# Kernel optimization log

Hardware: AMD Instinct MI355X
Metric: run time of the kernel (lower is better)

The kernel has to match this reference:

```python
import jax, jax.numpy as jnp
import numpy as np

NUM_LAYER, BS, NUM_HEADS, INPUT_LEN, ENC_LEN = 4, 2, 16, 1024, 588
HID = 256
LN_EPS = 1e-5


def _ln(x, g, b):
    mu = jnp.mean(x, axis=-1, keepdims=True)
    var = jnp.mean((x - mu) ** 2, axis=-1, keepdims=True)
    return (x - mu) / jnp.sqrt(var + LN_EPS) * g + b


def _mlp(x, Ws, bs, gs, betas):
    # 3-layer LayerNorm -> Linear (+GELU except last)
    n = len(Ws)
    for i in range(n):
        x = _ln(x, gs[i], betas[i])
        x = x @ Ws[i] + bs[i]
        if i < n - 1:
            x = jax.nn.gelu(x, approximate=False)  # torch F.gelu default = exact
    return x


def setup_inputs() -> dict:
    key = jax.random.key(0)
    ks = jax.random.split(key, 24)
    s = 0.02
    dims = [(ENC_LEN, HID), (HID, HID), (HID, 4)]
    inp = {
        "heatmap": jax.random.normal(ks[0], (NUM_LAYER, BS, NUM_HEADS, INPUT_LEN, ENC_LEN), jnp.float32),
        "attention_valid_mask": jnp.ones((BS, INPUT_LEN), jnp.float32),
        "W_head": jax.random.normal(ks[1], (NUM_LAYER * NUM_HEADS, 1), jnp.float32) * s,
        "b_head": jnp.zeros((1,), jnp.float32),
        "W_keep": jax.random.normal(ks[2], (ENC_LEN, 1), jnp.float32) * s,
        "b_keep": jnp.zeros((1,), jnp.float32),
    }
    for br in (1, 2):
        for i, (di, do) in enumerate(dims):
            inp[f"W{br}_{i}"] = jax.random.normal(ks[3 + br * 4 + i], (di, do), jnp.float32) * s
            inp[f"b{br}_{i}"] = jnp.zeros((do,), jnp.float32)
    for i, d in enumerate([ENC_LEN, HID, HID]):
        inp[f"g{i}"] = jnp.ones((d,), jnp.float32)
        inp[f"beta{i}"] = jnp.zeros((d,), jnp.float32)
    return inp


def reference(heatmap, attention_valid_mask, W_head, b_head, W_keep, b_keep,
              W1_0, b1_0, W1_1, b1_1, W1_2, b1_2,
              W2_0, b2_0, W2_1, b2_1, W2_2, b2_2,
              g0, beta0, g1, beta1, g2, beta2):
    num_layer, bs, num_heads, input_len, enc_len = heatmap.shape
    # [L,B,H,T,E] -> [B,T,E,L*H]
    hm = jnp.transpose(heatmap, (1, 3, 4, 0, 2)).reshape(bs, input_len, enc_len, num_layer * num_heads)
    x = (hm @ W_head + b_head)[..., 0]            # [B,T,E]
    x = x.reshape(bs * input_len, enc_len)        # [B*T, 588]
    logits_keep_row = (x @ W_keep + b_keep)[:, 0]  # [B*T]

    gs, betas = [g0, g1, g2], [beta0, beta1, beta2]
    out1 = _mlp(x, [W1_0, W1_1, W1_2], [b1_0, b1_1, b1_2], gs, betas)
    out2 = _mlp(x, [W2_0, W2_1, W2_2], [b2_0, b2_1, b2_2], gs, betas)
    keep = (jax.nn.sigmoid(logits_keep_row) > 0.5)[:, None]  # keep_row_thres = 0.5
    out = jnp.where(keep, out1, out2)             # gather/compute/scatter == select

    out = jax.nn.sigmoid(out.reshape(bs, input_len, 4))
    # input_len != 4095, so the mask-shift branch is skipped
    out = out * attention_valid_mask[:, :, None]
    x1, y1, w, h = out[:, :, 0], out[:, :, 1], out[:, :, 2], out[:, :, 3]
    return (x1, y1, x1 + w, y1 + h, logits_keep_row)
```

## Files before the change

### kernel.cpp

```cpp
#include <hip/hip_runtime.h>
#include <hip/hip_bf16.h>
#include <math.h>

#define NLAYER 4
#define BSZ 2
#define NHEADS 16
#define ILEN 1024
#define ELEN 588
#define HID 256
#define NROWS (BSZ * ILEN)
#define NCH (NLAYER * NHEADS)
#define S_H ((size_t)(ILEN) * ELEN)
#define S_B ((size_t)NHEADS * S_H)
#define S_L ((size_t)BSZ * S_B)

typedef float f32x4 __attribute__((ext_vector_type(4)));

__device__ __forceinline__ float gelu_exact(float x) {
    return 0.5f * x * (1.0f + erff(x * 0.70710678118654752440f));
}
__device__ __forceinline__ float sigmoidf(float x) {
    return 1.0f / (1.0f + expf(-x));
}
__device__ __forceinline__ float wave_sum(float v) {
    #pragma unroll
    for (int m = 1; m < 64; m <<= 1) v += __shfl_xor(v, m);
    return v;
}

__global__ __launch_bounds__(256) void k_reduce_ln0(
    const float* __restrict__ hm, const float* __restrict__ Wh,
    const float* __restrict__ bh, const float* __restrict__ Wk,
    const float* __restrict__ bk, const float* __restrict__ g0,
    const float* __restrict__ be0, float* __restrict__ y,
    float* __restrict__ out_logits)
{
    const int row = blockIdx.x;
    const int b = row >> 10;
    const int i = row & 1023;
    const int tid = threadIdx.x;

    __shared__ float s_wh[NCH];
    __shared__ float s_wk[ELEN];
    __shared__ float s_red[12];
    __shared__ float s_bcast[2];

    if (tid < NCH) s_wh[tid] = Wh[tid];
    for (int e = tid; e < ELEN; e += 256) s_wk[e] = Wk[e];
    __syncthreads();

    const int f4 = tid;
    f32x4 acc = {0.f, 0.f, 0.f, 0.f};

    if (f4 < 147) {
        const float* rowbase = hm + (size_t)b * S_B + (size_t)i * ELEN + (size_t)(f4 * 4);
        #pragma unroll 16
        for (int ch = 0; ch < NCH; ++ch) {
            const size_t off = (size_t)(ch >> 4) * S_L + (size_t)(ch & 15) * S_H;
            const f32x4 v = __builtin_nontemporal_load((const f32x4*)(rowbase + off));
            acc += v * s_wh[ch];
        }
        const float bhv = bh[0];
        acc.x += bhv; acc.y += bhv; acc.z += bhv; acc.w += bhv;
    }

    float sx = 0.f, sxx = 0.f, sk = 0.f;
    if (f4 < 147) {
        sx  = acc.x + acc.y + acc.z + acc.w;
        sxx = acc.x * acc.x + acc.y * acc.y + acc.z * acc.z + acc.w * acc.w;
        const float4 wk = *(const float4*)&s_wk[f4 * 4];
        sk  = acc.x * wk.x + acc.y * wk.y + acc.z * wk.z + acc.w * wk.w;
    }
    #pragma unroll
    for (int off = 32; off; off >>= 1) {
        sx  += __shfl_down(sx, off);
        sxx += __shfl_down(sxx, off);
        sk  += __shfl_down(sk, off);
    }
    const int wid = tid >> 6, lane = tid & 63;
    if (lane == 0) { s_red[wid] = sx; s_red[4 + wid] = sxx; s_red[8 + wid] = sk; }
    __syncthreads();
    if (tid == 0) {
        sx  = s_red[0] + s_red[1] + s_red[2] + s_red[3];
        sxx = s_red[4] + s_red[5] + s_red[6] + s_red[7];
        sk  = s_red[8] + s_red[9] + s_red[10] + s_red[11];
        const float mu   = sx * (1.0f / ELEN);
        const float var  = sxx * (1.0f / ELEN) - mu * mu;
        const float rstd = rsqrtf(var + 1e-5f);
        s_bcast[0] = mu; s_bcast[1] = rstd;
        out_logits[row] = sk + bk[0];
    }
    __syncthreads();
    if (f4 < 147) {
        const float mu = s_bcast[0], rstd = s_bcast[1];
        const float4 gv = *(const float4*)&g0[f4 * 4];
        const float4 bv = *(const float4*)&be0[f4 * 4];
        float4 o;
        o.x = (acc.x - mu) * rstd * gv.x + bv.x;
        o.y = (acc.y - mu) * rstd * gv.y + bv.y;
        o.z = (acc.z - mu) * rstd * gv.z + bv.z;
        o.w = (acc.w - mu) * rstd * gv.w + bv.w;
        *(float4*)&y[(size_t)row * ELEN + f4 * 4] = o;
    }
}

__global__ __launch_bounds__(512) void k_mlp_fused(
    const float* __restrict__ y,
    const float* __restrict__ W10, const float* __restrict__ b10,
    const float* __restrict__ W11, const float* __restrict__ b11,
    const float* __restrict__ W12, const float* __restrict__ b12,
    const float* __restrict__ W20, const float* __restrict__ b20,
    const float* __restrict__ W21, const float* __restrict__ b21,
    const float* __restrict__ W22, const float* __restrict__ b22,
    const float* __restrict__ g1, const float* __restrict__ be1,
    const float* __restrict__ g2, const float* __restrict__ be2,
    const float* __restrict__ mask, float* __restrict__ dout)
{
    __shared__ float y_lds[8][ELEN];
    __shared__ float h_lds[8][HID];

    const int tid  = threadIdx.x;
    const int row0 = blockIdx.x * 8;

    for (int fi = tid; fi < 8 * 147; fi += 512) {
        const int r = fi / 147, t = fi % 147;
        *(float4*)&y_lds[r][t * 4] =
            *(const float4*)&y[(size_t)(row0 + r) * ELEN + t * 4];
    }
    __syncthreads();

    const int w    = tid >> 6;
    const int lane = tid & 63;
    const int col  = lane * 4;
    const int grow = row0 + w;

    const float4 gg1 = *(const float4*)&g1[col];
    const float4 be1v = *(const float4*)&be1[col];
    const float4 gg2 = *(const float4*)&g2[col];
    const float4 be2v = *(const float4*)&be2[col];

    float res[2][4];

    #pragma unroll
    for (int br = 0; br < 2; ++br) {
        const float* W0  = br ? W20 : W10;
        const float* bb0 = br ? b20 : b10;
        const float* W1  = br ? W21 : W11;
        const float* bb1 = br ? b21 : b11;
        const float* W2  = br ? W22 : W12;
        const float* bb2 = br ? b22 : b12;

        float4 a = make_float4(0.f, 0.f, 0.f, 0.f);
        for (int e = 0; e < ELEN; e += 4) {
            const float4 ya = *(const float4*)&y_lds[w][e];
            const float4 w0 = *(const float4*)&W0[(size_t)(e + 0) * HID + col];
            const float4 w1 = *(const float4*)&W0[(size_t)(e + 1) * HID + col];
            const float4 w2 = *(const float4*)&W0[(size_t)(e + 2) * HID + col];
            const float4 w3 = *(const float4*)&W0[(size_t)(e + 3) * HID + col];
            a.x += ya.x * w0.x + ya.y * w1.x + ya.z * w2.x + ya.w * w3.x;
            a.y += ya.x * w0.y + ya.y * w1.y + ya.z * w2.y + ya.w * w3.y;
            a.z += ya.x * w0.z + ya.y * w1.z + ya.z * w2.z + ya.w * w3.z;
            a.w += ya.x * w0.w + ya.y * w1.w + ya.z * w2.w + ya.w * w3.w;
        }
        {
            const float4 bv = *(const float4*)&bb0[col];
            a.x = gelu_exact(a.x + bv.x);
            a.y = gelu_exact(a.y + bv.y);
            a.z = gelu_exact(a.z + bv.z);
            a.w = gelu_exact(a.w + bv.w);
        }
        {
            float s1 = wave_sum(a.x + a.y + a.z + a.w);
            float s2 = wave_sum(a.x * a.x + a.y * a.y + a.z * a.z + a.w * a.w);
            const float mu   = s1 * (1.0f / HID);
            const float rstd = rsqrtf(s2 * (1.0f / HID) - mu * mu + 1e-5f);
            float4 o;
            o.x = (a.x - mu) * rstd * gg1.x + be1v.x;
            o.y = (a.y - mu) * rstd * gg1.y + be1v.y;
            o.z = (a.z - mu) * rstd * gg1.z + be1v.z;
            o.w = (a.w - mu) * rstd * gg1.w + be1v.w;
            *(float4*)&h_lds[w][col] = o;
        }
        float4 c = make_float4(0.f, 0.f, 0.f, 0.f);
        for (int e = 0; e < HID; e += 4) {
            const float4 ha = *(const float4*)&h_lds[w][e];
            const float4 w0 = *(const float4*)&W1[(size_t)(e + 0) * HID + col];
            const float4 w1 = *(const float4*)&W1[(size_t)(e + 1) * HID + col];
            const float4 w2 = *(const float4*)&W1[(size_t)(e + 2) * HID + col];
            const float4 w3 = *(const float4*)&W1[(size_t)(e + 3) * HID + col];
            c.x += ha.x * w0.x + ha.y * w1.x + ha.z * w2.x + ha.w * w3.x;
            c.y += ha.x * w0.y + ha.y * w1.y + ha.z * w2.y + ha.w * w3.y;
            c.z += ha.x * w0.z + ha.y * w1.z + ha.z * w2.z + ha.w * w3.z;
            c.w += ha.x * w0.w + ha.y * w1.w + ha.z * w2.w + ha.w * w3.w;
        }
        {
            const float4 bv = *(const float4*)&bb1[col];
            c.x = gelu_exact(c.x + bv.x);
            c.y = gelu_exact(c.y + bv.y);
            c.z = gelu_exact(c.z + bv.z);
            c.w = gelu_exact(c.w + bv.w);
        }
        float zn[4];
        {
            float s1 = wave_sum(c.x + c.y + c.z + c.w);
            float s2 = wave_sum(c.x * c.x + c.y * c.y + c.z * c.z + c.w * c.w);
            const float mu   = s1 * (1.0f / HID);
            const float rstd = rsqrtf(s2 * (1.0f / HID) - mu * mu + 1e-5f);
            zn[0] = (c.x - mu) * rstd * gg2.x + be2v.x;
            zn[1] = (c.y - mu) * rstd * gg2.y + be2v.y;
            zn[2] = (c.z - mu) * rstd * gg2.z + be2v.z;
            zn[3] = (c.w - mu) * rstd * gg2.w + be2v.w;
        }
        float p[4] = {0.f, 0.f, 0.f, 0.f};
        #pragma unroll
        for (int k = 0; k < 4; ++k) {
            const float4 w4 = *(const float4*)&W2[(size_t)(col + k) * 4];
            p[0] += zn[k] * w4.x;
            p[1] += zn[k] * w4.y;
            p[2] += zn[k] * w4.z;
            p[3] += zn[k] * w4.w;
        }
        #pragma unroll
        for (int cc = 0; cc < 4; ++cc)
            res[br][cc] = wave_sum(p[cc]) + bb2[cc];
    }

    if (lane == 0) {
        const float logit = dout[4 * NROWS + grow];
        const float m = mask[grow];
        const float* sel = (logit > 0.f) ? res[0] : res[1];
        const float x1 = sigmoidf(sel[0]) * m;
        const float y1 = sigmoidf(sel[1]) * m;
        const float ww = sigmoidf(sel[2]) * m;
        const float hh = sigmoidf(sel[3]) * m;
        dout[grow]             = x1;
        dout[NROWS + grow]     = y1;
        dout[2 * NROWS + grow] = x1 + ww;
        dout[3 * NROWS + grow] = y1 + hh;
    }
}

extern "C" void kernel_launch(void* const* d_in, const int* in_sizes, int n_in,
                              void* d_out, int out_size, void* d_ws, size_t ws_size,
                              hipStream_t stream)
{
    const float* hm   = (const float*)d_in[0];
    const float* mask = (const float*)d_in[1];
    const float* Wh   = (const float*)d_in[2];
    const float* bh   = (const float*)d_in[3];
    const float* Wk   = (const float*)d_in[4];
    const float* bk   = (const float*)d_in[5];
    const float* W10  = (const float*)d_in[6];
    const float* b10  = (const float*)d_in[7];
    const float* W11  = (const float*)d_in[8];
    const float* b11  = (const float*)d_in[9];
    const float* W12  = (const float*)d_in[10];
    const float* b12  = (const float*)d_in[11];
    const float* W20  = (const float*)d_in[12];
    const float* b20  = (const float*)d_in[13];
    const float* W21  = (const float*)d_in[14];
    const float* b21  = (const float*)d_in[15];
    const float* W22  = (const float*)d_in[16];
    const float* b22  = (const float*)d_in[17];
    const float* g0   = (const float*)d_in[18];
    const float* be0  = (const float*)d_in[19];
    const float* g1   = (const float*)d_in[20];
    const float* be1  = (const float*)d_in[21];
    const float* g2   = (const float*)d_in[22];
    const float* be2  = (const float*)d_in[23];

    float* ws   = (float*)d_ws;
    float* y    = ws;
    float* dout = (float*)d_out;

    k_reduce_ln0<<<NROWS, 256, 0, stream>>>(hm, Wh, bh, Wk, bk, g0, be0,
                                            y, dout + 4 * NROWS);
    k_mlp_fused<<<NROWS / 8, 512, 0, stream>>>(y, W10, b10, W11, b11, W12, b12,
                                               W20, b20, W21, b21, W22, b22,
                                               g1, be1, g2, be2, mask, dout);
}
```

Before: 547.7 us.

## Process four rows per reduce block, split MLP branches with LDS weight tiles

The reduction kernel now handles four contiguous rows per 640-thread block. This gives each channel load a contiguous 4-row span and cuts the number of blocks, with cross-row statistics gathered through shared-memory partials. The MLP kernel is split so each block computes a single branch for 8 rows, staging weight tiles in LDS and having each wave compute two rows to reuse weights. A third small kernel does the keep/select, sigmoid and masking, at the cost of an extra launch and workspace round trip.

```diff
diff --git a/kernel.cpp b/kernel.cpp
--- a/kernel.cpp
+++ b/kernel.cpp
@@ -28,216 +28,251 @@
     return v;
 }
 
-__global__ __launch_bounds__(256) void k_reduce_ln0(
+__global__ __launch_bounds__(640) void k_reduce_ln0(
     const float* __restrict__ hm, const float* __restrict__ Wh,
     const float* __restrict__ bh, const float* __restrict__ Wk,
     const float* __restrict__ bk, const float* __restrict__ g0,
     const float* __restrict__ be0, float* __restrict__ y,
     float* __restrict__ out_logits)
 {
-    const int row = blockIdx.x;
-    const int b = row >> 10;
-    const int i = row & 1023;
-    const int tid = threadIdx.x;
+    const int row0 = blockIdx.x * 4;
+    const int b    = row0 >> 10;
+    const int i0   = row0 & 1023;
+    const int tid  = threadIdx.x;
 
     __shared__ float s_wh[NCH];
     __shared__ float s_wk[ELEN];
-    __shared__ float s_red[12];
-    __shared__ float s_bcast[2];
+    __shared__ float p_sx[588], p_sxx[588], p_sk[588];
+    __shared__ float s_stat[4][2];
 
     if (tid < NCH) s_wh[tid] = Wh[tid];
-    for (int e = tid; e < ELEN; e += 256) s_wk[e] = Wk[e];
+    for (int e = tid; e < ELEN; e += 640) s_wk[e] = Wk[e];
     __syncthreads();
 
-    const int f4 = tid;
+    const int q = tid;
     f32x4 acc = {0.f, 0.f, 0.f, 0.f};
-
-    if (f4 < 147) {
-        const float* rowbase = hm + (size_t)b * S_B + (size_t)i * ELEN + (size_t)(f4 * 4);
-        #pragma unroll 16
+    int r = 0, e4 = 0;
+
+    if (q < 588) {
+        r  = q / 147;
+        e4 = q - r * 147;
+        const f32x4* base = (const f32x4*)(hm + (size_t)b * S_B + (size_t)i0 * ELEN) + q;
+        #pragma unroll 8
         for (int ch = 0; ch < NCH; ++ch) {
-            const size_t off = (size_t)(ch >> 4) * S_L + (size_t)(ch & 15) * S_H;
-            const f32x4 v = __builtin_nontemporal_load((const f32x4*)(rowbase + off));
+            const size_t off4 = ((size_t)(ch >> 4) * S_L + (size_t)(ch & 15) * S_H) >> 2;
+            const f32x4 v = __builtin_nontemporal_load(base + off4);
             acc += v * s_wh[ch];
         }
         const float bhv = bh[0];
         acc.x += bhv; acc.y += bhv; acc.z += bhv; acc.w += bhv;
-    }
-
-    float sx = 0.f, sxx = 0.f, sk = 0.f;
-    if (f4 < 147) {
-        sx  = acc.x + acc.y + acc.z + acc.w;
-        sxx = acc.x * acc.x + acc.y * acc.y + acc.z * acc.z + acc.w * acc.w;
-        const float4 wk = *(const float4*)&s_wk[f4 * 4];
-        sk  = acc.x * wk.x + acc.y * wk.y + acc.z * wk.z + acc.w * wk.w;
-    }
-    #pragma unroll
-    for (int off = 32; off; off >>= 1) {
-        sx  += __shfl_down(sx, off);
-        sxx += __shfl_down(sxx, off);
-        sk  += __shfl_down(sk, off);
-    }
-    const int wid = tid >> 6, lane = tid & 63;
-    if (lane == 0) { s_red[wid] = sx; s_red[4 + wid] = sxx; s_red[8 + wid] = sk; }
+
+        const f32x4 wk = *(const f32x4*)&s_wk[e4 * 4];
+        p_sx[q]  = acc.x + acc.y + acc.z + acc.w;
+        p_sxx[q] = acc.x * acc.x + acc.y * acc.y + acc.z * acc.z + acc.w * acc.w;
+        p_sk[q]  = acc.x * wk.x + acc.y * wk.y + acc.z * wk.z + acc.w * wk.w;
+    }
     __syncthreads();
-    if (tid == 0) {
-        sx  = s_red[0] + s_red[1] + s_red[2] + s_red[3];
-        sxx = s_red[4] + s_red[5] + s_red[6] + s_red[7];
-        sk  = s_red[8] + s_red[9] + s_red[10] + s_red[11];
-        const float mu   = sx * (1.0f / ELEN);
-        const float var  = sxx * (1.0f / ELEN) - mu * mu;
-        const float rstd = rsqrtf(var + 1e-5f);
-        s_bcast[0] = mu; s_bcast[1] = rstd;
-        out_logits[row] = sk + bk[0];
+
+    const int w    = tid >> 6;
+    const int lane = tid & 63;
+    if (w < 4) {
+        float rsx = 0.f, rsxx = 0.f, rsk = 0.f;
+        for (int j = w * 147 + lane; j < w * 147 + 147; j += 64) {
+            rsx  += p_sx[j];
+            rsxx += p_sxx[j];
+            rsk  += p_sk[j];
+        }
+        rsx  = wave_sum(rsx);
+        rsxx = wave_sum(rsxx);
+        rsk  = wave_sum(rsk);
+        if (lane == 0) {
+            const float mu   = rsx * (1.0f / ELEN);
+            const float var  = rsxx * (1.0f / ELEN) - mu * mu;
+            s_stat[w][0] = mu;
+            s_stat[w][1] = rsqrtf(var + 1e-5f);
+            out_logits[row0 + w] = rsk + bk[0];
+        }
     }
     __syncthreads();
-    if (f4 < 147) {
-        const float mu = s_bcast[0], rstd = s_bcast[1];
-        const float4 gv = *(const float4*)&g0[f4 * 4];
-        const float4 bv = *(const float4*)&be0[f4 * 4];
-        float4 o;
+
+    if (q < 588) {
+        const float mu   = s_stat[r][0];
+        const float rstd = s_stat[r][1];
+        const f32x4 gv = *(const f32x4*)&g0[e4 * 4];
+        const f32x4 bv = *(const f32x4*)&be0[e4 * 4];
+        f32x4 o;
         o.x = (acc.x - mu) * rstd * gv.x + bv.x;
         o.y = (acc.y - mu) * rstd * gv.y + bv.y;
         o.z = (acc.z - mu) * rstd * gv.z + bv.z;
         o.w = (acc.w - mu) * rstd * gv.w + bv.w;
-        *(float4*)&y[(size_t)row * ELEN + f4 * 4] = o;
-    }
-}
-
-__global__ __launch_bounds__(512) void k_mlp_fused(
+        *((f32x4*)(y + (size_t)row0 * ELEN) + q) = o;
+    }
+}
+
+__global__ __launch_bounds__(256) void k_mlp_branch(
     const float* __restrict__ y,
-    const float* __restrict__ W10, const float* __restrict__ b10,
-    const float* __restrict__ W11, const float* __restrict__ b11,
-    const float* __restrict__ W12, const float* __restrict__ b12,
-    const float* __restrict__ W20, const float* __restrict__ b20,
-    const float* __restrict__ W21, const float* __restrict__ b21,
-    const float* __restrict__ W22, const float* __restrict__ b22,
+    const float* __restrict__ W0a, const float* __restrict__ b0a,
+    const float* __restrict__ W1a, const float* __restrict__ b1a,
+    const float* __restrict__ W2a, const float* __restrict__ b2a,
+    const float* __restrict__ W0b, const float* __restrict__ b0b,
+    const float* __restrict__ W1b, const float* __restrict__ b1b,
+    const float* __restrict__ W2b, const float* __restrict__ b2b,
     const float* __restrict__ g1, const float* __restrict__ be1,
     const float* __restrict__ g2, const float* __restrict__ be2,
-    const float* __restrict__ mask, float* __restrict__ dout)
+    float* __restrict__ res1, float* __restrict__ res2)
 {
     __shared__ float y_lds[8][ELEN];
+    __shared__ float w_lds[42 * HID];
     __shared__ float h_lds[8][HID];
 
+    const int bid  = blockIdx.x;
+    const int br   = bid >> 8;
+    const int rb   = bid & 255;
+    const int row0 = rb * 8;
     const int tid  = threadIdx.x;
-    const int row0 = blockIdx.x * 8;
-
-    for (int fi = tid; fi < 8 * 147; fi += 512) {
-        const int r = fi / 147, t = fi % 147;
-        *(float4*)&y_lds[r][t * 4] =
-            *(const float4*)&y[(size_t)(row0 + r) * ELEN + t * 4];
-    }
-    __syncthreads();
+
+    const float* W0 = br ? W0b : W0a;
+    const float* b0 = br ? b0b : b0a;
+    const float* W1 = br ? W1b : W1a;
+    const float* b1 = br ? b1b : b1a;
+    const float* W2 = br ? W2b : W2a;
+    const float* b2 = br ? b2b : b2a;
+    float*      res = br ? res2 : res1;
+
+    for (int fi = tid; fi < 8 * 147; fi += 256) {
+        const int r = fi / 147, t = fi - r * 147;
+        *(f32x4*)&y_lds[r][t * 4] =
+            *((const f32x4*)(y + (size_t)(row0 + r) * ELEN) + t);
+    }
 
     const int w    = tid >> 6;
     const int lane = tid & 63;
     const int col  = lane * 4;
-    const int grow = row0 + w;
-
-    const float4 gg1 = *(const float4*)&g1[col];
-    const float4 be1v = *(const float4*)&be1[col];
-    const float4 gg2 = *(const float4*)&g2[col];
-    const float4 be2v = *(const float4*)&be2[col];
-
-    float res[2][4];
-
-    #pragma unroll
-    for (int br = 0; br < 2; ++br) {
-        const float* W0  = br ? W20 : W10;
-        const float* bb0 = br ? b20 : b10;
-        const float* W1  = br ? W21 : W11;
-        const float* bb1 = br ? b21 : b11;
-        const float* W2  = br ? W22 : W12;
-        const float* bb2 = br ? b22 : b12;
-
-        float4 a = make_float4(0.f, 0.f, 0.f, 0.f);
-        for (int e = 0; e < ELEN; e += 4) {
-            const float4 ya = *(const float4*)&y_lds[w][e];
-            const float4 w0 = *(const float4*)&W0[(size_t)(e + 0) * HID + col];
-            const float4 w1 = *(const float4*)&W0[(size_t)(e + 1) * HID + col];
-            const float4 w2 = *(const float4*)&W0[(size_t)(e + 2) * HID + col];
-            const float4 w3 = *(const float4*)&W0[(size_t)(e + 3) * HID + col];
-            a.x += ya.x * w0.x + ya.y * w1.x + ya.z * w2.x + ya.w * w3.x;
-            a.y += ya.x * w0.y + ya.y * w1.y + ya.z * w2.y + ya.w * w3.y;
-            a.z += ya.x * w0.z + ya.y * w1.z + ya.z * w2.z + ya.w * w3.z;
-            a.w += ya.x * w0.w + ya.y * w1.w + ya.z * w2.w + ya.w * w3.w;
-        }
-        {
-            const float4 bv = *(const float4*)&bb0[col];
-            a.x = gelu_exact(a.x + bv.x);
-            a.y = gelu_exact(a.y + bv.y);
-            a.z = gelu_exact(a.z + bv.z);
-            a.w = gelu_exact(a.w + bv.w);
-        }
-        {
-            float s1 = wave_sum(a.x + a.y + a.z + a.w);
-            float s2 = wave_sum(a.x * a.x + a.y * a.y + a.z * a.z + a.w * a.w);
+    const int lr0  = 2 * w, lr1 = 2 * w + 1;
+
+    f32x4 a0 = {0.f, 0.f, 0.f, 0.f};
+    f32x4 a1 = {0.f, 0.f, 0.f, 0.f};
+    for (int c = 0; c < 14; ++c) {
+        const int k0 = c * 42;
+        __syncthreads();
+        for (int fi = tid; fi < 42 * 64; fi += 256)
+            ((f32x4*)w_lds)[fi] =
+                *((const f32x4*)(W0 + (size_t)(k0 + (fi >> 6)) * HID) + (fi & 63));
+        __syncthreads();
+        #pragma unroll
+        for (int e = 0; e < 42; e += 2) {
+            const f32x4 w0 = *(const f32x4*)&w_lds[(e + 0) * HID + col];
+            const f32x4 w1 = *(const f32x4*)&w_lds[(e + 1) * HID + col];
+            const float2 ya = *(const float2*)&y_lds[lr0][k0 + e];
+            const float2 yb = *(const float2*)&y_lds[lr1][k0 + e];
+            a0 += w0 * ya.x + w1 * ya.y;
+            a1 += w0 * yb.x + w1 * yb.y;
+        }
+    }
+
+    {
+        const f32x4 bv  = *(const f32x4*)&b0[col];
+        const f32x4 gg  = *(const f32x4*)&g1[col];
+        const f32x4 bb  = *(const f32x4*)&be1[col];
+        #pragma unroll
+        for (int rr = 0; rr < 2; ++rr) {
+            f32x4 v = rr ? a1 : a0;
+            v.x = gelu_exact(v.x + bv.x);
+            v.y = gelu_exact(v.y + bv.y);
+            v.z = gelu_exact(v.z + bv.z);
+            v.w = gelu_exact(v.w + bv.w);
+            const float s1 = wave_sum(v.x + v.y + v.z + v.w);
+            const float s2 = wave_sum(v.x * v.x + v.y * v.y + v.z * v.z + v.w * v.w);
             const float mu   = s1 * (1.0f / HID);
             const float rstd = rsqrtf(s2 * (1.0f / HID) - mu * mu + 1e-5f);
-            float4 o;
-            o.x = (a.x - mu) * rstd * gg1.x + be1v.x;
-            o.y = (a.y - mu) * rstd * gg1.y + be1v.y;
-            o.z = (a.z - mu) * rstd * gg1.z + be1v.z;
-            o.w = (a.w - mu) * rstd * gg1.w + be1v.w;
-            *(float4*)&h_lds[w][col] = o;
-        }
-        float4 c = make_float4(0.f, 0.f, 0.f, 0.f);
-        for (int e = 0; e < HID; e += 4) {
-            const float4 ha = *(const float4*)&h_lds[w][e];
-            const float4 w0 = *(const float4*)&W1[(size_t)(e + 0) * HID + col];
-            const float4 w1 = *(const float4*)&W1[(size_t)(e + 1) * HID + col];
-            const float4 w2 = *(const float4*)&W1[(size_t)(e + 2) * HID + col];
-            const float4 w3 = *(const float4*)&W1[(size_t)(e + 3) * HID + col];
-            c.x += ha.x * w0.x + ha.y * w1.x + ha.z * w2.x + ha.w * w3.x;
-            c.y += ha.x * w0.y + ha.y * w1.y + ha.z * w2.y + ha.w * w3.y;
-            c.z += ha.x * w0.z + ha.y * w1.z + ha.z * w2.z + ha.w * w3.z;
-            c.w += ha.x * w0.w + ha.y * w1.w + ha.z * w2.w + ha.w * w3.w;
-        }
-        {
-            const float4 bv = *(const float4*)&bb1[col];
-            c.x = gelu_exact(c.x + bv.x);
-            c.y = gelu_exact(c.y + bv.y);
-            c.z = gelu_exact(c.z + bv.z);
-            c.w = gelu_exact(c.w + bv.w);
-        }
-        float zn[4];
-        {
-            float s1 = wave_sum(c.x + c.y + c.z + c.w);
-            float s2 = wave_sum(c.x * c.x + c.y * c.y + c.z * c.z + c.w * c.w);
+            f32x4 o;
+            o.x = (v.x - mu) * rstd * gg.x + bb.x;
+            o.y = (v.y - mu) * rstd * gg.y + bb.y;
+            o.z = (v.z - mu) * rstd * gg.z + bb.z;
+            o.w = (v.w - mu) * rstd * gg.w + bb.w;
+            *(f32x4*)&h_lds[rr ? lr1 : lr0][col] = o;
+        }
+    }
+
+    f32x4 c0 = {0.f, 0.f, 0.f, 0.f};
+    f32x4 c1 = {0.f, 0.f, 0.f, 0.f};
+    for (int c = 0; c < 8; ++c) {
+        const int k0 = c * 32;
+        __syncthreads();
+        for (int fi = tid; fi < 32 * 64; fi += 256)
+            ((f32x4*)w_lds)[fi] =
+                *((const f32x4*)(W1 + (size_t)(k0 + (fi >> 6)) * HID) + (fi & 63));
+        __syncthreads();
+        #pragma unroll
+        for (int e = 0; e < 32; e += 2) {
+            const f32x4 w0 = *(const f32x4*)&w_lds[(e + 0) * HID + col];
+            const f32x4 w1 = *(const f32x4*)&w_lds[(e + 1) * HID + col];
+            const float2 ha = *(const float2*)&h_lds[lr0][k0 + e];
+            const float2 hb = *(const float2*)&h_lds[lr1][k0 + e];
+            c0 += w0 * ha.x + w1 * ha.y;
+            c1 += w0 * hb.x + w1 * hb.y;
+        }
+    }
+
+    {
+        const f32x4 bv = *(const f32x4*)&b1[col];
+        const f32x4 gg = *(const f32x4*)&g2[col];
+        const f32x4 bb = *(const f32x4*)&be2[col];
+        #pragma unroll
+        for (int rr = 0; rr < 2; ++rr) {
+            f32x4 v = rr ? c1 : c0;
+            v.x = gelu_exact(v.x + bv.x);
+            v.y = gelu_exact(v.y + bv.y);
+            v.z = gelu_exact(v.z + bv.z);
+            v.w = gelu_exact(v.w + bv.w);
+            const float s1 = wave_sum(v.x + v.y + v.z + v.w);
+            const float s2 = wave_sum(v.x * v.x + v.y * v.y + v.z * v.z + v.w * v.w);
             const float mu   = s1 * (1.0f / HID);
             const float rstd = rsqrtf(s2 * (1.0f / HID) - mu * mu + 1e-5f);
-            zn[0] = (c.x - mu) * rstd * gg2.x + be2v.x;
-            zn[1] = (c.y - mu) * rstd * gg2.y + be2v.y;
-            zn[2] = (c.z - mu) * rstd * gg2.z + be2v.z;
-            zn[3] = (c.w - mu) * rstd * gg2.w + be2v.w;
-        }
-        float p[4] = {0.f, 0.f, 0.f, 0.f};
-        #pragma unroll
-        for (int k = 0; k < 4; ++k) {
-            const float4 w4 = *(const float4*)&W2[(size_t)(col + k) * 4];
-            p[0] += zn[k] * w4.x;
-            p[1] += zn[k] * w4.y;
-            p[2] += zn[k] * w4.z;
-            p[3] += zn[k] * w4.w;
-        }
-        #pragma unroll
-        for (int cc = 0; cc < 4; ++cc)
-            res[br][cc] = wave_sum(p[cc]) + bb2[cc];
-    }
-
-    if (lane == 0) {
-        const float logit = dout[4 * NROWS + grow];
-        const float m = mask[grow];
-        const float* sel = (logit > 0.f) ? res[0] : res[1];
-        const float x1 = sigmoidf(sel[0]) * m;
-        const float y1 = sigmoidf(sel[1]) * m;
-        const float ww = sigmoidf(sel[2]) * m;
-        const float hh = sigmoidf(sel[3]) * m;
-        dout[grow]             = x1;
-        dout[NROWS + grow]     = y1;
-        dout[2 * NROWS + grow] = x1 + ww;
-        dout[3 * NROWS + grow] = y1 + hh;
-    }
+            float zn[4];
+            zn[0] = (v.x - mu) * rstd * gg.x + bb.x;
+            zn[1] = (v.y - mu) * rstd * gg.y + bb.y;
+            zn[2] = (v.z - mu) * rstd * gg.z + bb.z;
+            zn[3] = (v.w - mu) * rstd * gg.w + bb.w;
+
+            float p[4] = {0.f, 0.f, 0.f, 0.f};
+            #pragma unroll
+            for (int k = 0; k < 4; ++k) {
+                const f32x4 w4 = *(const f32x4*)&W2[(size_t)(col + k) * 4];
+                p[0] += zn[k] * w4.x;
+                p[1] += zn[k] * w4.y;
+                p[2] += zn[k] * w4.z;
+                p[3] += zn[k] * w4.w;
+            }
+            f32x4 out;
+            out.x = wave_sum(p[0]) + b2[0];
+            out.y = wave_sum(p[1]) + b2[1];
+            out.z = wave_sum(p[2]) + b2[2];
+            out.w = wave_sum(p[3]) + b2[3];
+            if (lane == 0)
+                *(f32x4*)&res[(size_t)(row0 + (rr ? lr1 : lr0)) * 4] = out;
+        }
+    }
+}
+
+__global__ __launch_bounds__(256) void k_select(
+    const float* __restrict__ res1, const float* __restrict__ res2,
+    const float* __restrict__ mask, float* __restrict__ dout)
+{
+    const int row = blockIdx.x * 256 + threadIdx.x;
+    if (row >= NROWS) return;
+    const float logit = dout[4 * NROWS + row];
+    const float m = mask[row];
+    const f32x4 s = (logit > 0.f) ? *(const f32x4*)&res1[(size_t)row * 4]
+                                  : *(const f32x4*)&res2[(size_t)row * 4];
+    const float x1 = sigmoidf(s.x) * m;
+    const float y1 = sigmoidf(s.y) * m;
+    const float ww = sigmoidf(s.z) * m;
+    const float hh = sigmoidf(s.w) * m;
+    dout[row]             = x1;
+    dout[NROWS + row]     = y1;
+    dout[2 * NROWS + row] = x1 + ww;
+    dout[3 * NROWS + row] = y1 + hh;
 }
 
 extern "C" void kernel_launch(void* const* d_in, const int* in_sizes, int n_in,
@@ -271,11 +306,15 @@
 
     float* ws   = (float*)d_ws;
     float* y    = ws;
+    float* res1 = y + (size_t)NROWS * ELEN;
+    float* res2 = res1 + (size_t)NROWS * 4;
     float* dout = (float*)d_out;
 
-    k_reduce_ln0<<<NROWS, 256, 0, stream>>>(hm, Wh, bh, Wk, bk, g0, be0,
-                                            y, dout + 4 * NROWS);
-    k_mlp_fused<<<NROWS / 8, 512, 0, stream>>>(y, W10, b10, W11, b11, W12, b12,
-                                               W20, b20, W21, b21, W22, b22,
-                                               g1, be1, g2, be2, mask, dout);
-}
+    k_reduce_ln0<<<NROWS / 4, 640, 0, stream>>>(hm, Wh, bh, Wk, bk, g0, be0,
+                                                y, dout + 4 * NROWS);
+    k_mlp_branch<<<512, 256, 0, stream>>>(y,
+                                          W10, b10, W11, b11, W12, b12,
+                                          W20, b20, W21, b21, W22, b22,
+                                          g1, be1, g2, be2, res1, res2);
+    k_select<<<NROWS / 256, 256, 0, stream>>>(res1, res2, mask, dout);
+}
```

Result: no change. 538.3 us (-1.7%).
